# Optimization experiments

Hardware: AMD Instinct MI355X
Metric: run time of the kernel (lower is better)

The kernel has to match this reference:

```python
import jax, jax.numpy as jnp
import numpy as np

N = 50000      # nodes
E = 500000     # edges (avg degree 10)
D_IN = 256     # input feature dim
HID = 256      # hidden_channels
HEADS = 8
C_HID = HID // HEADS   # 32 per-head dim for concat layers
NCLS = 8               # num_classes (last layer per-head dim, concat=False)


def setup_inputs() -> dict:
    key = jax.random.key(0)
    keys = iter(jax.random.split(key, 64))
    def w(shape, s=0.05):
        return jax.random.normal(next(keys), shape, jnp.float32) * s
    inp = {}
    inp["x"] = jax.random.normal(next(keys), (N, D_IN), jnp.float32)
    inp["edge_index"] = jax.random.randint(next(keys), (2, E), 0, N, jnp.int32)
    # (fan_in, heads*per_head_out, skip_out) per layer; layer3: concat=False
    layer_cfg = [(D_IN, HEADS * C_HID, HEADS * C_HID),
                 (HID, HEADS * C_HID, HEADS * C_HID),
                 (HID, HEADS * NCLS, NCLS)]
    for i, (fin, hc, skip) in enumerate(layer_cfg, 1):
        for nm in ("q", "k", "v"):
            inp[f"W{nm}{i}"] = w((fin, hc))
            inp[f"b{nm}{i}"] = jnp.zeros((hc,), jnp.float32)
        inp[f"Ws{i}"] = w((fin, skip))
        inp[f"bs{i}"] = jnp.zeros((skip,), jnp.float32)
        inp[f"Wb{i}"] = w((3 * skip, 1))
    for i in (1, 2):
        inp[f"ln{i}_g"] = jnp.ones((HID,), jnp.float32)
        inp[f"ln{i}_b"] = jnp.zeros((HID,), jnp.float32)
    return inp


def _layer_norm(x, g, b):
    mu = x.mean(-1, keepdims=True)
    var = ((x - mu) ** 2).mean(-1, keepdims=True)
    return (x - mu) * jax.lax.rsqrt(var + 1e-5) * g + b


def _tconv(x, src, dst, Wq, bq, Wk, bk, Wv, bv, Ws, bs, Wb, concat):
    """PyG TransformerConv with beta=True, root_weight=True, eval-mode (no dropout)."""
    n = x.shape[0]
    q = (x @ Wq + bq).reshape(n, HEADS, -1)   # [N,H,C]
    k = (x @ Wk + bk).reshape(n, HEADS, -1)
    v = (x @ Wv + bv).reshape(n, HEADS, -1)
    C = q.shape[-1]
    # per-edge attention logits, scaled dot product
    logits = (q[dst] * k[src]).sum(-1) * jax.lax.rsqrt(jnp.float32(C))  # [E,H]
    # segment softmax over incoming edges of each dst node
    m = jax.ops.segment_max(logits, dst, num_segments=n)                # [N,H]
    m = jnp.where(jnp.isfinite(m), m, 0.0)                              # empty segments
    e = jnp.exp(logits - m[dst])
    s = jax.ops.segment_sum(e, dst, num_segments=n)
    alpha = e / (s[dst] + 1e-16)                                        # [E,H]
    # scatter-aggregate messages
    out = jax.ops.segment_sum(v[src] * alpha[:, :, None], dst, num_segments=n)  # [N,H,C]
    out = out.reshape(n, -1) if concat else out.mean(axis=1)
    # beta-gated skip connection
    xr = x @ Ws + bs
    beta = jax.nn.sigmoid(jnp.concatenate([out, xr, out - xr], axis=-1) @ Wb)   # [N,1]
    return beta * xr + (1.0 - beta) * out


def reference(x, edge_index,
              Wq1, bq1, Wk1, bk1, Wv1, bv1, Ws1, bs1, Wb1,
              Wq2, bq2, Wk2, bk2, Wv2, bv2, Ws2, bs2, Wb2,
              Wq3, bq3, Wk3, bk3, Wv3, bv3, Ws3, bs3, Wb3,
              ln1_g, ln1_b, ln2_g, ln2_b):
    src, dst = edge_index[0], edge_index[1]
    h = jax.nn.relu(_layer_norm(
        _tconv(x, src, dst, Wq1, bq1, Wk1, bk1, Wv1, bv1, Ws1, bs1, Wb1, True),
        ln1_g, ln1_b))
    h = jax.nn.relu(_layer_norm(
        _tconv(h, src, dst, Wq2, bq2, Wk2, bk2, Wv2, bv2, Ws2, bs2, Wb2, True),
        ln2_g, ln2_b))
    return _tconv(h, src, dst, Wq3, bq3, Wk3, bk3, Wv3, bv3, Ws3, bs3, Wb3, False)
```

## Files before the change

kernel.cpp:

```cpp
#include <hip/hip_runtime.h>
#include <stdint.h>

typedef __attribute__((ext_vector_type(8))) short short8;
typedef __attribute__((ext_vector_type(4))) float f32x4;
typedef __attribute__((ext_vector_type(4))) _Float16 half4;
typedef __attribute__((ext_vector_type(2))) _Float16 half2v;
typedef __attribute__((ext_vector_type(4))) int i32x4;

struct us4 { unsigned short x, y, z, w; };

__device__ __forceinline__ float b2f(unsigned short u){
  union { unsigned int i; float f; } x; x.i = ((unsigned int)u) << 16; return x.f;
}
__device__ __forceinline__ unsigned short f2b(float f){
  union { float f; unsigned int i; } x; x.f = f;
  unsigned int i = x.i;
  unsigned int r = (i + 0x7FFFu + ((i >> 16) & 1u)) >> 16;
  return (unsigned short)r;
}
__device__ __forceinline__ unsigned short f2h(float f){
  _Float16 h = (_Float16)f;
  union { _Float16 h; unsigned short u; } c; c.h = h; return c.u;
}
__device__ __forceinline__ float sane(float v){
  return fminf(fmaxf(v, -1e30f), 1e30f);
}
__device__ __forceinline__ float lclamp(float v){
  return fminf(fmaxf(v, -60.f), 60.f);
}
__device__ __forceinline__ float ldin(const void* p, size_t i, int f32){
  return f32 ? ((const float*)p)[i] : b2f(((const unsigned short*)p)[i]);
}
__device__ __forceinline__ float dot4h(half2v a0, half2v a1, half2v b0, half2v b1){
#if __has_builtin(__builtin_amdgcn_fdot2)
  return __builtin_amdgcn_fdot2(a0, b0, __builtin_amdgcn_fdot2(a1, b1, 0.f, false), false);
#else
  return (float)a0.x*(float)b0.x + (float)a0.y*(float)b0.y
       + (float)a1.x*(float)b1.x + (float)a1.y*(float)b1.y;
#endif
}
__device__ __forceinline__ void gload_lds16(const void* g, void* l){
  __builtin_amdgcn_global_load_lds(
      (const __attribute__((address_space(1))) void*)g,
      (__attribute__((address_space(3))) void*)l, 16, 0, 0);
}

__global__ void k_flag(const unsigned short* __restrict__ xu, int* __restrict__ flag){
  __shared__ int cnt;
  if (threadIdx.x == 0) cnt = 0;
  __syncthreads();
  unsigned u = xu[2 * threadIdx.x];
  int e = (u >> 7) & 0xFF;
  if (e >= 97 && e <= 132) atomicAdd(&cnt, 1);
  __syncthreads();
  if (threadIdx.x == 0) flag[0] = (cnt >= 192) ? 0 : 1;
}

__global__ void k_cvt(const void* __restrict__ xin, unsigned short* __restrict__ xb,
                      int n4, const int* __restrict__ flagp){
  int f32 = *flagp;
  int i = blockIdx.x * 256 + threadIdx.x;
  if (i < n4){
    if (f32){
      float4 v = ((const float4*)xin)[i];
      us4 o = { f2b(v.x), f2b(v.y), f2b(v.z), f2b(v.w) };
      ((us4*)xb)[i] = o;
    } else {
      ((us4*)xb)[i] = ((const us4*)xin)[i];
    }
  }
}

__global__ void k_deg(const int* __restrict__ ei, int E, int N, int* __restrict__ deg){
  int e = blockIdx.x * 256 + threadIdx.x;
  if (e < E){
    unsigned d = (unsigned)ei[E + e];
    if (d < (unsigned)N) atomicAdd(&deg[d], 1);
  }
}

__device__ __forceinline__ int pad4(int d){ return (d + 3) & ~3; }

__global__ void k_bsum(const int* __restrict__ deg, int N, int* __restrict__ bsum){
  int b = blockIdx.x, t = threadIdx.x;
  int i0 = b * 1024 + t * 4;
  int s = 0;
  if (i0 + 4 <= N){
    int4 v = *(const int4*)&deg[i0];
    s = pad4(v.x) + pad4(v.y) + pad4(v.z) + pad4(v.w);
  } else {
    #pragma unroll
    for (int j = 0; j < 4; ++j){ int i = i0 + j; if (i < N) s += pad4(deg[i]); }
  }
  #pragma unroll
  for (int off = 32; off; off >>= 1) s += __shfl_xor(s, off);
  __shared__ int ws[4];
  if ((t & 63) == 0) ws[t >> 6] = s;
  __syncthreads();
  if (t == 0) bsum[b] = ws[0] + ws[1] + ws[2] + ws[3];
}

__global__ void k_bscan(const int* __restrict__ bsum, int nb,
                        int* __restrict__ boff, int* __restrict__ rowptr, int N){
  int t = threadIdx.x;
  if (nb <= 64){
    int v = (t < nb) ? bsum[t] : 0;
    int inc = v;
    #pragma unroll
    for (int off = 1; off < 64; off <<= 1){
      int u = __shfl_up(inc, off);
      if (t >= off) inc += u;
    }
    if (t < nb) boff[t] = inc - v;
    if (t == 63) rowptr[N] = inc;
  } else {
    if (t == 0){
      int run = 0;
      for (int i = 0; i < nb; ++i){ boff[i] = run; run += bsum[i]; }
      rowptr[N] = run;
    }
  }
}

__global__ void k_rowptr(const int* __restrict__ deg, const int* __restrict__ boff,
                         int N, int* __restrict__ rowptr, int* __restrict__ cursor){
  int b = blockIdx.x, t = threadIdx.x;
  int i0 = b * 1024 + t * 4;
  int d0 = 0, d1 = 0, d2 = 0, d3 = 0;
  if (i0 + 4 <= N){
    int4 v = *(const int4*)&deg[i0];
    d0 = v.x; d1 = v.y; d2 = v.z; d3 = v.w;
  } else {
    if (i0     < N) d0 = deg[i0];
    if (i0 + 1 < N) d1 = deg[i0 + 1];
    if (i0 + 2 < N) d2 = deg[i0 + 2];
    if (i0 + 3 < N) d3 = deg[i0 + 3];
  }
  int p0 = pad4(d0), p1 = pad4(d1), p2 = pad4(d2), p3 = pad4(d3);
  int s = p0 + p1 + p2 + p3;
  int lane = t & 63, w = t >> 6;
  int inc = s;
  #pragma unroll
  for (int off = 1; off < 64; off <<= 1){
    int u = __shfl_up(inc, off);
    if (lane >= off) inc += u;
  }
  int wex = inc - s;
  __shared__ int wtot[4];
  if (lane == 63) wtot[w] = inc;
  __syncthreads();
  int cross = 0;
  for (int i = 0; i < w; ++i) cross += wtot[i];
  int basev = boff[b] + cross + wex;
  int r0 = basev, r1 = basev + p0, r2 = r1 + p1, r3 = r2 + p2;
  if (i0 + 4 <= N){
    int4 o = { r0, r1, r2, r3 };
    *(int4*)&rowptr[i0] = o;
    *(int4*)&cursor[i0] = o;
  } else {
    if (i0     < N){ rowptr[i0]   = r0; cursor[i0]   = r0; }
    if (i0 + 1 < N){ rowptr[i0+1] = r1; cursor[i0+1] = r1; }
    if (i0 + 2 < N){ rowptr[i0+2] = r2; cursor[i0+2] = r2; }
    if (i0 + 3 < N){ rowptr[i0+3] = r3; cursor[i0+3] = r3; }
  }
}

__global__ void k_scatter(const int* __restrict__ ei, int E, int N, int Epad,
                          int* __restrict__ cursor, int* __restrict__ srcs){
  int e = blockIdx.x * 256 + threadIdx.x;
  if (e < E){
    unsigned d = (unsigned)ei[E + e];
    if (d < (unsigned)N){
      int pos = atomicAdd(&cursor[d], 1);
      if ((unsigned)pos < (unsigned)Epad){
        unsigned s = (unsigned)ei[e];
        srcs[pos] = (s < (unsigned)N) ? (int)(s * 1024u) : 0;
      }
    }
  }
}

__global__ void k_pack(const void* __restrict__ Wq, const void* __restrict__ bq,
                       const void* __restrict__ Wk, const void* __restrict__ bk,
                       const void* __restrict__ Wv, const void* __restrict__ bv,
                       const void* __restrict__ Ws, const void* __restrict__ bs,
                       unsigned short* __restrict__ WT, float* __restrict__ bias,
                       int Mq, int Ms, int K, const int* __restrict__ flagp){
  int f32 = *flagp;
  int cg = blockIdx.x;
  int k  = threadIdx.x;
  int mat, c, mc;
  if (cg < 3 * Mq){ mat = cg / Mq; c = cg % Mq; mc = Mq; }
  else if (cg < 3 * Mq + Ms){ mat = 3; c = cg - 3 * Mq; mc = Ms; }
  else { mat = 4; c = 0; mc = 1; }
  const void* W = (mat==0)?Wq:(mat==1)?Wk:(mat==2)?Wv:(mat==3)?Ws:(const void*)0;
  WT[(size_t)cg * K + k] = (mat < 4) ? f2b(ldin(W, (size_t)k * mc + c, f32)) : (unsigned short)0;
  if (k == 0){
    const void* B = (mat==0)?bq:(mat==1)?bk:(mat==2)?bv:(mat==3)?bs:(const void*)0;
    bias[cg] = (mat < 4) ? ldin(B, c, f32) : 0.f;
  }
}

__global__ __launch_bounds__(256) void k_gemm(const unsigned short* __restrict__ A,
                                              const unsigned short* __restrict__ WT,
                                              const float* __restrict__ bias,
                                              unsigned short* __restrict__ qout,
                                              char* __restrict__ kvout,
                                              unsigned short* __restrict__ xout,
                                              int N, int Mout, int secshift){
  __shared__ __align__(16) unsigned short sh[64*32 + 256*32];
  unsigned short* Achk = sh;
  unsigned short* Blds = sh + 64*32;
  auto Clds = (unsigned short(*)[276])sh;
  int tid = threadIdx.x, wid = tid >> 6, lane = tid & 63;
  int l15 = lane & 15, l4 = lane >> 4;
  int nit = Mout >> 8;
  int it = blockIdx.x % nit;
  int row0 = (blockIdx.x / nit) * 64;
  int secw = 1 << secshift;
  int sec, blk;
  if (nit == 1){ sec = wid; blk = 0; }
  else if (it == 0){ sec = 0; blk = wid; }
  else if (it == 3){ sec = 3; blk = wid; }
  else { sec = (wid < 2) ? 1 : 2; blk = (it - 1) * 2 + (wid & 1); }
  int cbf = sec * secw + blk * 64;

  int sr = lane >> 2, sc = lane & 3;
  int arow = row0 + wid * 16 + sr; if (arow >= N) arow = N - 1;
  const unsigned short* Ag = A + (size_t)arow * 256 + sc * 8;
  const unsigned short* Bg[4];
  #pragma unroll
  for (int j = 0; j < 4; ++j){
    int r = wid * 64 + j * 16 + sr;
    int gcol;
    if (nit == 1 || it == 0) gcol = r;
    else if (it == 3)        gcol = 768 + r;
    else if (it == 1)        gcol = r + (r < 128 ? 256 : 384);
    else                     gcol = r + (r < 128 ? 384 : 512);
    Bg[j] = WT + (size_t)gcol * 256 + sc * 8;
  }
  unsigned short* AldsD = Achk + (wid * 16) * 32;
  unsigned short* BldsD = Blds + (wid * 64) * 32;

  f32x4 acc[4][4] = {};
  for (int k0 = 0; k0 < 256; k0 += 32){
    gload_lds16(Ag + k0, AldsD);
    gload_lds16(Bg[0] + k0, BldsD);
    gload_lds16(Bg[1] + k0, BldsD + 16*32);
    gload_lds16(Bg[2] + k0, BldsD + 32*32);
    gload_lds16(Bg[3] + k0, BldsD + 48*32);
    __syncthreads();
    short8 a0 = *(const short8*)&Achk[(     l15)*32 + l4*8];
    short8 a1 = *(const short8*)&Achk[(16 + l15)*32 + l4*8];
    short8 a2 = *(const short8*)&Achk[(32 + l15)*32 + l4*8];
    short8 a3 = *(const short8*)&Achk[(48 + l15)*32 + l4*8];
    short8 b0 = *(const short8*)&Blds[(wid*64      + l15)*32 + l4*8];
    short8 b1 = *(const short8*)&Blds[(wid*64 + 16 + l15)*32 + l4*8];
    short8 b2 = *(const short8*)&Blds[(wid*64 + 32 + l15)*32 + l4*8];
    short8 b3 = *(const short8*)&Blds[(wid*64 + 48 + l15)*32 + l4*8];
    acc[0][0] = __builtin_amdgcn_mfma_f32_16x16x32_bf16(a0, b0, acc[0][0], 0,0,0);
    acc[0][1] = __builtin_amdgcn_mfma_f32_16x16x32_bf16(a0, b1, acc[0][1], 0,0,0);
    acc[0][2] = __builtin_amdgcn_mfma_f32_16x16x32_bf16(a0, b2, acc[0][2], 0,0,0);
    acc[0][3] = __builtin_amdgcn_mfma_f32_16x16x32_bf16(a0, b3, acc[0][3], 0,0,0);
    acc[1][0] = __builtin_amdgcn_mfma_f32_16x16x32_bf16(a1, b0, acc[1][0], 0,0,0);
    acc[1][1] = __builtin_amdgcn_mfma_f32_16x16x32_bf16(a1, b1, acc[1][1], 0,0,0);
    acc[1][2] = __builtin_amdgcn_mfma_f32_16x16x32_bf16(a1, b2, acc[1][2], 0,0,0);
    acc[1][3] = __builtin_amdgcn_mfma_f32_16x16x32_bf16(a1, b3, acc[1][3], 0,0,0);
    acc[2][0] = __builtin_amdgcn_mfma_f32_16x16x32_bf16(a2, b0, acc[2][0], 0,0,0);
    acc[2][1] = __builtin_amdgcn_mfma_f32_16x16x32_bf16(a2, b1, acc[2][1], 0,0,0);
    acc[2][2] = __builtin_amdgcn_mfma_f32_16x16x32_bf16(a2, b2, acc[2][2], 0,0,0);
    acc[2][3] = __builtin_amdgcn_mfma_f32_16x16x32_bf16(a2, b3, acc[2][3], 0,0,0);
    acc[3][0] = __builtin_amdgcn_mfma_f32_16x16x32_bf16(a3, b0, acc[3][0], 0,0,0);
    acc[3][1] = __builtin_amdgcn_mfma_f32_16x16x32_bf16(a3, b1, acc[3][1], 0,0,0);
    acc[3][2] = __builtin_amdgcn_mfma_f32_16x16x32_bf16(a3, b2, acc[3][2], 0,0,0);
    acc[3][3] = __builtin_amdgcn_mfma_f32_16x16x32_bf16(a3, b3, acc[3][3], 0,0,0);
    __syncthreads();
  }
  int strow = tid >> 3, stchunk = tid & 7;
  #pragma unroll
  for (int ph = 0; ph < 2; ++ph){
    #pragma unroll
    for (int rt2 = 0; rt2 < 2; ++rt2){
      int rt = ph*2 + rt2;
      #pragma unroll
      for (int ct = 0; ct < 4; ++ct){
        float bv = bias[cbf + ct*16 + l15];
        #pragma unroll
        for (int r = 0; r < 4; ++r)
          Clds[rt2*16 + l4*4 + r][wid*64 + ct*16 + l15] = f2h(acc[rt][ct][r] + bv);
      }
    }
    __syncthreads();
    int grow = row0 + ph*32 + strow;
    if (grow < N){
      if (nit == 4){
        if (it == 0 || it == 3){
          unsigned short* Bp = (it == 0) ? qout : xout;
          int g0 = stchunk * 32;
          unsigned short* dst = Bp + (size_t)grow * secw + g0;
          const unsigned short* srcp = &Clds[strow][g0];
          #pragma unroll
          for (int j = 0; j < 4; ++j)
            *(short8*)(dst + j*8) = *(const short8*)(srcp + j*8);
        } else {
          int secbase = (it == 1) ? 0 : 128;
          int scl = stchunk * 16;
          char* dstb = kvout + (size_t)grow * 1024 + (size_t)(secbase + scl) * 4;
          const unsigned short* kp = &Clds[strow][scl];
          const unsigned short* vp = &Clds[strow][128 + scl];
          #pragma unroll
          for (int g2 = 0; g2 < 4; ++g2){
            union { unsigned long long u[2]; i32x4 v; } st;
            st.u[0] = *(const unsigned long long*)(kp + g2*4);
            st.u[1] = *(const unsigned long long*)(vp + g2*4);
            *(i32x4*)(dstb + g2*16) = st.v;
          }
        }
      } else {
        if (stchunk < 2){
          int g0 = stchunk * 32;
          unsigned short* dst = qout + (size_t)grow * secw + g0;
          const unsigned short* srcp = &Clds[strow][g0];
          #pragma unroll
          for (int j = 0; j < 4; ++j)
            *(short8*)(dst + j*8) = *(const short8*)(srcp + j*8);
        } else if (stchunk < 6){
          int scl = (stchunk - 2) * 16;
          char* dstb = kvout + (size_t)grow * 256 + (size_t)scl * 4;
          const unsigned short* kp = &Clds[strow][64 + scl];
          const unsigned short* vp = &Clds[strow][128 + scl];
          #pragma unroll
          for (int g2 = 0; g2 < 4; ++g2){
            union { unsigned long long u[2]; i32x4 v; } st;
            st.u[0] = *(const unsigned long long*)(kp + g2*4);
            st.u[1] = *(const unsigned long long*)(vp + g2*4);
            *(i32x4*)(dstb + g2*16) = st.v;
          }
        } else {
          int g0 = (stchunk - 6) * 32;
          unsigned short* dst = xout + (size_t)grow * secw + g0;
          const unsigned short* srcp = &Clds[strow][192 + g0];
          #pragma unroll
          for (int j = 0; j < 4; ++j)
            *(short8*)(dst + j*8) = *(const short8*)(srcp + j*8);
        }
      }
    }
    __syncthreads();
  }
}

__global__ __launch_bounds__(256) void k_attn(const unsigned short* __restrict__ qb,
                                              const char* __restrict__ kvb,
                                              const unsigned short* __restrict__ xb,
                                              const int* __restrict__ rowptr,
                                              const int* __restrict__ degv,
                                              const int* __restrict__ srcs,
                                              const void* __restrict__ Wb,
                                              const void* __restrict__ lng,
                                              const void* __restrict__ lnb,
                                              unsigned short* __restrict__ hout,
                                              int N, int E, const int* __restrict__ flagp){
  int f32 = *flagp;
  int tid = threadIdx.x, w = tid >> 6, l = tid & 63;
  int n = blockIdx.x * 4 + w;
  if (n >= N) return;
  unsigned lof = (unsigned)l * 16u;
  size_t nbase = (size_t)n * 512;
  union KV { i32x4 v; _Float16 h[8]; half2v h2[4]; };
  half4 qv = *(const half4*)((const char*)qb + nbase + (unsigned)l * 8u);
  half2v q01 = { qv.x, qv.y }, q23 = { qv.z, qv.w };
  int e0 = rowptr[n]; if (e0 < 0) e0 = 0;
  int dg = degv[n]; if (dg < 0) dg = 0; if (dg > E) dg = E;
  int npad = (dg + 3) & ~3;
  const float scale = 0.17677669529663687f;
  float ss = 0.f, o0 = 0.f, o1 = 0.f, o2 = 0.f, o3 = 0.f;

  auto consume = [&](const KV& kv, int valid){
    float p = dot4h(q01, q23, kv.h2[0], kv.h2[1]);
    p += __shfl_xor(p, 1); p += __shfl_xor(p, 2); p += __shfl_xor(p, 4);
    float a = valid ? __expf(lclamp(p * scale)) : 0.f;
    ss += a;
    o0 += a * (float)kv.h[4];
    o1 += a * (float)kv.h[5];
    o2 += a * (float)kv.h[6];
    o3 += a * (float)kv.h[7];
  };

  if (npad > 0){
    i32x4 offs = *(const i32x4*)&srcs[e0];
    KV c0, c1, c2, c3;
    c0.v = *(const i32x4*)(kvb + (unsigned)offs[0] + lof);
    c1.v = *(const i32x4*)(kvb + (unsigned)offs[1] + lof);
    c2.v = *(const i32x4*)(kvb + (unsigned)offs[2] + lof);
    c3.v = *(const i32x4*)(kvb + (unsigned)offs[3] + lof);
    int base = 0;
    #pragma unroll 1
    for (; base + 4 < npad; base += 4){
      i32x4 offsN = *(const i32x4*)&srcs[e0 + base + 4];
      KV n0, n1, n2, n3;
      n0.v = *(const i32x4*)(kvb + (unsigned)offsN[0] + lof);
      n1.v = *(const i32x4*)(kvb + (unsigned)offsN[1] + lof);
      n2.v = *(const i32x4*)(kvb + (unsigned)offsN[2] + lof);
      n3.v = *(const i32x4*)(kvb + (unsigned)offsN[3] + lof);
      consume(c0, 1); consume(c1, 1); consume(c2, 1); consume(c3, 1);
      c0 = n0; c1 = n1; c2 = n2; c3 = n3;
    }
    consume(c0, base + 0 < dg);
    consume(c1, base + 1 < dg);
    consume(c2, base + 2 < dg);
    consume(c3, base + 3 < dg);
  }

  float sinv = 1.f / (ss + 1e-16f);
  o0 = sane(o0 * sinv); o1 = sane(o1 * sinv);
  o2 = sane(o2 * sinv); o3 = sane(o3 * sinv);
  int c = l * 4;
  half4 xv = *(const half4*)((const char*)xb + nbase + (unsigned)l * 8u);
  float x0 = sane((float)xv.x), x1 = sane((float)xv.y);
  float x2 = sane((float)xv.z), x3 = sane((float)xv.w);
  float d = o0*ldin(Wb, c+0, f32) + x0*ldin(Wb, 256+c+0, f32) + (o0-x0)*ldin(Wb, 512+c+0, f32)
          + o1*ldin(Wb, c+1, f32) + x1*ldin(Wb, 256+c+1, f32) + (o1-x1)*ldin(Wb, 512+c+1, f32)
          + o2*ldin(Wb, c+2, f32) + x2*ldin(Wb, 256+c+2, f32) + (o2-x2)*ldin(Wb, 512+c+2, f32)
          + o3*ldin(Wb, c+3, f32) + x3*ldin(Wb, 256+c+3, f32) + (o3-x3)*ldin(Wb, 512+c+3, f32);
  #pragma unroll
  for (int off = 32; off; off >>= 1) d += __shfl_xor(d, off);
  float beta = 1.f / (1.f + __expf(-d));
  float r0 = beta*x0 + (1.f-beta)*o0;
  float r1 = beta*x1 + (1.f-beta)*o1;
  float r2 = beta*x2 + (1.f-beta)*o2;
  float r3 = beta*x3 + (1.f-beta)*o3;
  float sm = r0 + r1 + r2 + r3;
  #pragma unroll
  for (int off = 32; off; off >>= 1) sm += __shfl_xor(sm, off);
  float mu = sm * (1.f/256.f);
  float d0 = r0-mu, d1 = r1-mu, d2 = r2-mu, d3 = r3-mu;
  float vv2 = d0*d0 + d1*d1 + d2*d2 + d3*d3;
  #pragma unroll
  for (int off = 32; off; off >>= 1) vv2 += __shfl_xor(vv2, off);
  float rs = rsqrtf(vv2 * (1.f/256.f) + 1e-5f);
  us4 outv;
  outv.x = f2b(fmaxf(d0*rs*ldin(lng,c+0,f32) + ldin(lnb,c+0,f32), 0.f));
  outv.y = f2b(fmaxf(d1*rs*ldin(lng,c+1,f32) + ldin(lnb,c+1,f32), 0.f));
  outv.z = f2b(fmaxf(d2*rs*ldin(lng,c+2,f32) + ldin(lnb,c+2,f32), 0.f));
  outv.w = f2b(fmaxf(d3*rs*ldin(lng,c+3,f32) + ldin(lnb,c+3,f32), 0.f));
  *(us4*)&hout[(size_t)n * 256 + c] = outv;
}

__global__ __launch_bounds__(256) void k_final(const unsigned short* __restrict__ q3b,
                                               const char* __restrict__ kv3b,
                                               const unsigned short* __restrict__ x3b,
                                               const int* __restrict__ rowptr,
                                               const int* __restrict__ degv,
                                               const int* __restrict__ srcs,
                                               const void* __restrict__ Wb,
                                               void* __restrict__ outp,
                                               int N, int E, const int* __restrict__ flagp){
  int f32 = *flagp;
  int tid = threadIdx.x, w = tid >> 6, l = tid & 63;
  int n = blockIdx.x * 4 + w;
  if (n >= N) return;
  int es = l >> 4, g = l & 15, j = g & 1;
  unsigned lof = (unsigned)g * 16u;
  size_t nbase = (size_t)n * 128;
  union KV { i32x4 v; _Float16 h[8]; half2v h2[4]; };
  half4 qv = *(const half4*)((const char*)q3b + nbase + (unsigned)g * 8u);
  half2v q01 = { qv.x, qv.y }, q23 = { qv.z, qv.w };
  int e0 = rowptr[n]; if (e0 < 0) e0 = 0;
  int dg = degv[n]; if (dg < 0) dg = 0; if (dg > E) dg = E;
  int npad = (dg + 3) & ~3;
  const float scale = 0.35355339059327373f;
  float ss = 0.f, o0 = 0.f, o1 = 0.f, o2 = 0.f, o3 = 0.f;

  auto consume = [&](const KV& kv, int valid){
    float p = dot4h(q01, q23, kv.h2[0], kv.h2[1]);
    p += __shfl_xor(p, 1);
    float a = valid ? __expf(lclamp(p * scale)) : 0.f;
    ss += a;
    o0 += a * (float)kv.h[4];
    o1 += a * (float)kv.h[5];
    o2 += a * (float)kv.h[6];
    o3 += a * (float)kv.h[7];
  };

  int idx = es;
  if (idx < npad){
    KV c;
    c.v = *(const i32x4*)(kv3b + (((unsigned)srcs[e0 + idx]) >> 2) + lof);
    #pragma unroll 1
    for (; idx + 4 < npad; idx += 4){
      KV nx;
      nx.v = *(const i32x4*)(kv3b + (((unsigned)srcs[e0 + idx + 4]) >> 2) + lof);
      consume(c, idx < dg);
      c = nx;
    }
    consume(c, idx < dg);
  }
  #pragma unroll
  for (int off = 16; off <= 32; off <<= 1){
    ss += __shfl_xor(ss, off);
    o0 += __shfl_xor(o0, off); o1 += __shfl_xor(o1, off);
    o2 += __shfl_xor(o2, off); o3 += __shfl_xor(o3, off);
  }
  float sinv = 1.f / (ss + 1e-16f);
  o0 = sane(o0 * sinv); o1 = sane(o1 * sinv);
  o2 = sane(o2 * sinv); o3 = sane(o3 * sinv);
  #pragma unroll
  for (int off = 2; off <= 8; off <<= 1){
    o0 += __shfl_xor(o0, off); o1 += __shfl_xor(o1, off);
    o2 += __shfl_xor(o2, off); o3 += __shfl_xor(o3, off);
  }
  o0 *= 0.125f; o1 *= 0.125f; o2 *= 0.125f; o3 *= 0.125f;
  half4 xv = *(const half4*)((const char*)x3b + nbase + (unsigned)(j * 8));
  float x0 = sane((float)xv.x), x1 = sane((float)xv.y);
  float x2 = sane((float)xv.z), x3v = sane((float)xv.w);
  int c = j*4;
  float d = o0*ldin(Wb, c+0, f32) + x0*ldin(Wb, 8+c+0, f32) + (o0-x0)*ldin(Wb, 16+c+0, f32)
          + o1*ldin(Wb, c+1, f32) + x1*ldin(Wb, 8+c+1, f32) + (o1-x1)*ldin(Wb, 16+c+1, f32)
          + o2*ldin(Wb, c+2, f32) + x2*ldin(Wb, 8+c+2, f32) + (o2-x2)*ldin(Wb, 16+c+2, f32)
          + o3*ldin(Wb, c+3, f32) + x3v*ldin(Wb, 8+c+3, f32) + (o3-x3v)*ldin(Wb, 16+c+3, f32);
  d += __shfl_xor(d, 1);
  float beta = 1.f / (1.f + __expf(-d));
  float r0 = beta*x0  + (1.f-beta)*o0;
  float r1 = beta*x1  + (1.f-beta)*o1;
  float r2 = beta*x2  + (1.f-beta)*o2;
  float r3 = beta*x3v + (1.f-beta)*o3;
  if (l < 2){
    if (f32){
      float* op = (float*)outp + (size_t)n*8 + l*4;
      op[0] = r0; op[1] = r1; op[2] = r2; op[3] = r3;
    } else {
      unsigned short* op = (unsigned short*)outp + (size_t)n*8 + l*4;
      op[0] = f2b(r0); op[1] = f2b(r1); op[2] = f2b(r2); op[3] = f2b(r3);
    }
  }
}

extern "C" void kernel_launch(void* const* d_in, const int* in_sizes, int n_in,
                              void* d_out, int out_size, void* d_ws, size_t ws_size,
                              hipStream_t stream){
  const int* ei = (const int*)d_in[1];
  const int N = in_sizes[0] / 256;
  const int E = in_sizes[1] / 2;
  const int Epad = E + 4 * N + 64;

  char* wsp = (char*)d_ws;
  size_t off = 0;
  auto alloc = [&](size_t b) -> void* {
    void* p = wsp + off; off = (off + b + 255) & ~(size_t)255; return p;
  };
  unsigned short* WT1  = (unsigned short*)alloc((size_t)1024*256*2);
  unsigned short* WT2  = (unsigned short*)alloc((size_t)1024*256*2);
  unsigned short* WT3  = (unsigned short*)alloc((size_t)256*256*2);
  float* bias1 = (float*)alloc(1024*4);
  float* bias2 = (float*)alloc(1024*4);
  float* bias3 = (float*)alloc(256*4);
  int* flag   = (int*)alloc(256);
  int* deg    = (int*)alloc((size_t)N*4);
  int* rowptr = (int*)alloc((size_t)(N+1)*4);
  int* cursor = (int*)alloc((size_t)N*4);
  int* bsum   = (int*)alloc(1024*4);
  int* boff   = (int*)alloc(1024*4);
  int* srcs   = (int*)alloc((size_t)Epad*4);
  unsigned short* xbf = (unsigned short*)alloc((size_t)N*256*2);
  unsigned short* qb  = (unsigned short*)alloc((size_t)N*256*2);
  char*           kvb = (char*)alloc((size_t)N*1024);
  unsigned short* xb  = (unsigned short*)alloc((size_t)N*256*2);
  unsigned short* hbuf= (unsigned short*)alloc((size_t)N*256*2);
  (void)ws_size; (void)n_in; (void)out_size;

  k_flag<<<1, 256, 0, stream>>>((const unsigned short*)d_in[0], flag);
  int n4 = (N * 256) / 4;
  k_cvt<<<(n4 + 255) / 256, 256, 0, stream>>>(d_in[0], xbf, n4, flag);

  hipMemsetAsync(deg, 0, (size_t)N*4, stream);
  hipMemsetAsync(srcs, 0, (size_t)Epad*4, stream);
  int eb = (E + 255) / 256;
  int nbk = (N + 1023) / 1024;
  k_deg<<<eb, 256, 0, stream>>>(ei, E, N, deg);
  k_bsum<<<nbk, 256, 0, stream>>>(deg, N, bsum);
  k_bscan<<<1, 64, 0, stream>>>(bsum, nbk, boff, rowptr, N);
  k_rowptr<<<nbk, 256, 0, stream>>>(deg, boff, N, rowptr, cursor);
  k_scatter<<<eb, 256, 0, stream>>>(ei, E, N, Epad, cursor, srcs);

  k_pack<<<1024, 256, 0, stream>>>(d_in[2],  d_in[3],  d_in[4],  d_in[5],  d_in[6],  d_in[7],  d_in[8],  d_in[9],  WT1, bias1, 256, 256, 256, flag);
  k_pack<<<1024, 256, 0, stream>>>(d_in[11], d_in[12], d_in[13], d_in[14], d_in[15], d_in[16], d_in[17], d_in[18], WT2, bias2, 256, 256, 256, flag);
  k_pack<<< 256, 256, 0, stream>>>(d_in[20], d_in[21], d_in[22], d_in[23], d_in[24], d_in[25], d_in[26], d_in[27], WT3, bias3,  64,   8, 256, flag);

  int rb = (N + 63) / 64;
  int nb = (N + 3) / 4;
  k_gemm<<<rb * 4, 256, 0, stream>>>(xbf, WT1, bias1, qb, kvb, xb, N, 1024, 8);
  k_attn<<<nb, 256, 0, stream>>>(qb, kvb, xb, rowptr, deg, srcs, d_in[10], d_in[29], d_in[30], hbuf, N, E, flag);
  k_gemm<<<rb * 4, 256, 0, stream>>>(hbuf, WT2, bias2, qb, kvb, xb, N, 1024, 8);
  k_attn<<<nb, 256, 0, stream>>>(qb, kvb, xb, rowptr, deg, srcs, d_in[19], d_in[31], d_in[32], hbuf, N, E, flag);
  k_gemm<<<rb, 256, 0, stream>>>(hbuf, WT3, bias3, qb, kvb, xb, N, 256, 6);
  k_final<<<nb, 256, 0, stream>>>(qb, kvb, xb, rowptr, deg, srcs, d_in[28], d_out, N, E, flag);
}
```

Baseline: 595.2 us.

## Split each node's edge loop across two wavefronts in attention kernel

Each destination node in the attention kernel is now handled by two wavefronts instead of one. They take alternating groups of four edges, and their partial softmax sums and weighted accumulators are combined through shared memory before the gating and layernorm epilogue. The aim is to double memory-level parallelism on the gathered K/V loads and to shorten the serial per-node latency chain. In exchange it adds a block-wide barrier and an LDS reduction, and half the wavefronts sit idle during the epilogue. Because the logits are not max-subtracted, no rescaling is needed when merging the two halves.

```diff
diff --git a/kernel.cpp b/kernel.cpp
--- a/kernel.cpp
+++ b/kernel.cpp
@@ -361,18 +361,22 @@
                                               const void* __restrict__ lnb,
                                               unsigned short* __restrict__ hout,
                                               int N, int E, const int* __restrict__ flagp){
+  __shared__ f32x4 po[4][64];
+  __shared__ float pss[4][64];
   int f32 = *flagp;
   int tid = threadIdx.x, w = tid >> 6, l = tid & 63;
-  int n = blockIdx.x * 4 + w;
-  if (n >= N) return;
+  int half = w & 1;
+  int n = blockIdx.x * 2 + (w >> 1);
+  int nvalid = (n < N);
+  int nc = nvalid ? n : (N - 1);
   unsigned lof = (unsigned)l * 16u;
-  size_t nbase = (size_t)n * 512;
+  size_t nbase = (size_t)nc * 512;
   union KV { i32x4 v; _Float16 h[8]; half2v h2[4]; };
   half4 qv = *(const half4*)((const char*)qb + nbase + (unsigned)l * 8u);
   half2v q01 = { qv.x, qv.y }, q23 = { qv.z, qv.w };
-  int e0 = rowptr[n]; if (e0 < 0) e0 = 0;
-  int dg = degv[n]; if (dg < 0) dg = 0; if (dg > E) dg = E;
-  int npad = (dg + 3) & ~3;
+  int e0 = rowptr[nc]; if (e0 < 0) e0 = 0;
+  int dg = nvalid ? degv[nc] : 0; if (dg < 0) dg = 0; if (dg > E) dg = E;
+  int ngr = ((dg + 3) & ~3) >> 2;
   const float scale = 0.17677669529663687f;
   float ss = 0.f, o0 = 0.f, o1 = 0.f, o2 = 0.f, o3 = 0.f;
 
@@ -387,17 +391,17 @@
     o3 += a * (float)kv.h[7];
   };
 
-  if (npad > 0){
-    i32x4 offs = *(const i32x4*)&srcs[e0];
+  int g = half;
+  if (g < ngr){
+    i32x4 offs = *(const i32x4*)&srcs[e0 + g*4];
     KV c0, c1, c2, c3;
     c0.v = *(const i32x4*)(kvb + (unsigned)offs[0] + lof);
     c1.v = *(const i32x4*)(kvb + (unsigned)offs[1] + lof);
     c2.v = *(const i32x4*)(kvb + (unsigned)offs[2] + lof);
     c3.v = *(const i32x4*)(kvb + (unsigned)offs[3] + lof);
-    int base = 0;
     #pragma unroll 1
-    for (; base + 4 < npad; base += 4){
-      i32x4 offsN = *(const i32x4*)&srcs[e0 + base + 4];
+    for (; g + 2 < ngr; g += 2){
+      i32x4 offsN = *(const i32x4*)&srcs[e0 + (g + 2)*4];
       KV n0, n1, n2, n3;
       n0.v = *(const i32x4*)(kvb + (unsigned)offsN[0] + lof);
       n1.v = *(const i32x4*)(kvb + (unsigned)offsN[1] + lof);
@@ -406,11 +410,21 @@
       consume(c0, 1); consume(c1, 1); consume(c2, 1); consume(c3, 1);
       c0 = n0; c1 = n1; c2 = n2; c3 = n3;
     }
-    consume(c0, base + 0 < dg);
-    consume(c1, base + 1 < dg);
-    consume(c2, base + 2 < dg);
-    consume(c3, base + 3 < dg);
-  }
+    int b4 = g * 4;
+    consume(c0, b4 + 0 < dg);
+    consume(c1, b4 + 1 < dg);
+    consume(c2, b4 + 2 < dg);
+    consume(c3, b4 + 3 < dg);
+  }
+
+  po[w][l] = (f32x4){ o0, o1, o2, o3 };
+  pss[w][l] = ss;
+  __syncthreads();
+  if (half) return;
+  f32x4 op = po[w + 1][l];
+  ss += pss[w + 1][l];
+  o0 += op[0]; o1 += op[1]; o2 += op[2]; o3 += op[3];
+  if (!nvalid) return;
 
   float sinv = 1.f / (ss + 1e-16f);
   o0 = sane(o0 * sinv); o1 = sane(o1 * sinv);
@@ -588,11 +602,12 @@
   k_pack<<< 256, 256, 0, stream>>>(d_in[20], d_in[21], d_in[22], d_in[23], d_in[24], d_in[25], d_in[26], d_in[27], WT3, bias3,  64,   8, 256, flag);
 
   int rb = (N + 63) / 64;
+  int nb2 = (N + 1) / 2;
   int nb = (N + 3) / 4;
   k_gemm<<<rb * 4, 256, 0, stream>>>(xbf, WT1, bias1, qb, kvb, xb, N, 1024, 8);
-  k_attn<<<nb, 256, 0, stream>>>(qb, kvb, xb, rowptr, deg, srcs, d_in[10], d_in[29], d_in[30], hbuf, N, E, flag);
+  k_attn<<<nb2, 256, 0, stream>>>(qb, kvb, xb, rowptr, deg, srcs, d_in[10], d_in[29], d_in[30], hbuf, N, E, flag);
   k_gemm<<<rb * 4, 256, 0, stream>>>(hbuf, WT2, bias2, qb, kvb, xb, N, 1024, 8);
-  k_attn<<<nb, 256, 0, stream>>>(qb, kvb, xb, rowptr, deg, srcs, d_in[19], d_in[31], d_in[32], hbuf, N, E, flag);
+  k_attn<<<nb2, 256, 0, stream>>>(qb, kvb, xb, rowptr, deg, srcs, d_in[19], d_in[31], d_in[32], hbuf, N, E, flag);
   k_gemm<<<rb, 256, 0, stream>>>(hbuf, WT3, bias3, qb, kvb, xb, N, 256, 6);
   k_final<<<nb, 256, 0, stream>>>(qb, kvb, xb, rowptr, deg, srcs, d_in[28], d_out, N, E, flag);
 }
```

New measurement: 604.4 us. No clear change (+1.5%).
